# Kernel optimization log

Measured on AMD Instinct MI355X. Metric: run time of the kernel, lower is better.

The kernel has to match this reference:

```python
import jax, jax.numpy as jnp
import numpy as np

SEQ, D, HID, C = 512, 768, 128, 5
NENT, SPAN = 128, 16


def setup_inputs() -> dict:
    key = jax.random.key(0)
    ks = jax.random.split(key, 24)
    s = 0.02

    def rn(k, shape, scale=s):
        return jax.random.normal(k, shape, dtype=jnp.float32) * scale

    inp = {
        "encoder_output": rn(ks[0], (1, SEQ, D), 1.0),
        "holder_idxs": jax.random.randint(ks[1], (NENT, SPAN), 0, SEQ, dtype=jnp.int32),
        "target_idxs": jax.random.randint(ks[2], (NENT, SPAN), 0, SEQ, dtype=jnp.int32),
        "exp_idxs": jax.random.randint(ks[3], (NENT, SPAN), 0, SEQ, dtype=jnp.int32),
    }
    names = ["Wh_f", "bh_f", "Wh_b", "bh_b", "Wt_f", "bt_f", "Wt_b", "bt_b",
             "We_f", "be_f", "We_b", "be_b"]
    for n, k in zip(names, ks[4:16]):
        shape = (4 * HID, D) if n.startswith("W") else (4 * HID,)
        inp[n] = rn(k, shape)
    inp["T_he"] = rn(ks[16], (2 * HID, 2 * HID, 2 * HID))
    inp["T_te"] = rn(ks[17], (2 * HID, 2 * HID, 2 * HID))
    inp["T_cls"] = rn(ks[18], (2 * HID, C, 2 * HID))
    return inp


def _lstm_cell_step(x, W_ih, b):
    # Single LSTM step with h0=c0=0 (the torch module feeds seq_len=1 to nn.LSTM,
    # so W_hh @ h0 vanishes; b = b_ih + b_hh). Gate order: i, f, g, o.
    g = x @ W_ih.T + b                         # [n, L, 4H]
    i, f, gg, o = jnp.split(g, 4, axis=-1)
    c = jax.nn.sigmoid(i) * jnp.tanh(gg)
    return jax.nn.sigmoid(o) * jnp.tanh(c)     # h, [n, L, H]


def _lstm_pool(enc_seq, idxs, Wf, bf, Wb, bb):
    toks = enc_seq[idxs]                       # [n, L, D] gather
    h = jnp.concatenate([_lstm_cell_step(toks, Wf, bf),
                         _lstm_cell_step(toks, Wb, bb)], axis=-1)  # [n, L, 2H]
    return h.max(axis=1)                       # max-pool over span -> [n, 2H]


def reference(encoder_output, holder_idxs, target_idxs, exp_idxs,
              Wh_f, bh_f, Wh_b, bh_b, Wt_f, bt_f, Wt_b, bt_b,
              We_f, be_f, We_b, be_b, T_he, T_te, T_cls):
    enc = encoder_output[0]                    # [SEQ, D]
    He = _lstm_pool(enc, holder_idxs, Wh_f, bh_f, Wh_b, bh_b)   # [nh, 2H]
    Te = _lstm_pool(enc, target_idxs, Wt_f, bt_f, Wt_b, bt_b)   # [nt, 2H]
    Ee = _lstm_pool(enc, exp_idxs, We_f, be_f, We_b, be_b)      # [ne, 2H]

    # hep[i,k] = He[i] @ T_he @ Ee[k];  tep[j,k] = Te[j] @ T_te @ Ee[k]
    hep = jnp.einsum('ia,abc,kc->ikb', He, T_he, Ee)            # [nh, ne, 2H]
    tep = jnp.einsum('ja,abc,kc->jkb', Te, T_te, Ee)            # [nt, ne, 2H]
    # pred[i,j,k,m] = tep[j,k] @ T_cls[:,m,:] @ hep[i,k]
    pred = jnp.einsum('jkb,bmc,ikc->ijkm', tep, T_cls, hep)     # [nh, nt, ne, C]
    return pred
```

## Files before the change

kernel.cpp:

```cpp
#include <hip/hip_runtime.h>
#include <hip/hip_bf16.h>
#include <math.h>

#define DIM   768
#define HID   128
#define H2    256
#define NENT  128
#define SPAN  16
#define NCLS  5

#define POOLB_OFF 0
#define HEPB_OFF  196608
#define TEPB_OFF  (HEPB_OFF + 8388608)
#define TCLSB_OFF (TEPB_OFF + 8388608)
#define WB_OFF    (TCLSB_OFF + 655360)
#define TOKB_OFF  21168128
#define GATES_OFF (TOKB_OFF + 9437184)
#define TMP30_OFF 21168128
#define TMP31_OFF (TMP30_OFF + 16777216)
#define PREDT_OFF 21168128

typedef __attribute__((ext_vector_type(8))) short bf16x8;
typedef __attribute__((ext_vector_type(4))) float f32x4;

__device__ __forceinline__ float sigmoidf_(float x) { return 1.0f / (1.0f + __expf(-x)); }

__device__ __forceinline__ unsigned short f2bf(float x) {
    __hip_bfloat16 h = __float2bfloat16(x);
    return *reinterpret_cast<unsigned short*>(&h);
}

__global__ __launch_bounds__(256)
void prep_kernel(const float* __restrict__ Whf, const float* __restrict__ Whb,
                 const float* __restrict__ Wtf, const float* __restrict__ Wtb,
                 const float* __restrict__ Wef, const float* __restrict__ Web,
                 const float* __restrict__ Tcls, const float* __restrict__ enc,
                 const int* __restrict__ idx_h, const int* __restrict__ idx_t,
                 const int* __restrict__ idx_e,
                 unsigned short* __restrict__ WB, unsigned short* __restrict__ TB,
                 unsigned short* __restrict__ tokB)
{
    const int bb = blockIdx.x;
    const int tid = threadIdx.x;
    if (bb < 1728) {
        int gid = bb * 256 + tid;
        int t2  = gid / 73728;
        int rem = gid % 73728;
        int n   = rem / 192;
        int c4  = rem % 192;
        int gate = n >> 7, j = n & 127;
        int srow = (gate == 0) ? j : (gate == 1) ? 256 + j : 384 + j;
        const float* W = (t2 == 0) ? Whf : (t2 == 1) ? Whb : (t2 == 2) ? Wtf :
                         (t2 == 3) ? Wtb : (t2 == 4) ? Wef : Web;
        float4 v = ((const float4*)(W + srow * DIM))[c4];
        unsigned short* d = WB + ((size_t)(t2 * 384 + n)) * DIM + c4 * 4;
        d[0] = f2bf(v.x); d[1] = f2bf(v.y); d[2] = f2bf(v.z); d[3] = f2bf(v.w);
    } else if (bb < 3008) {
        int idx = (bb - 1728) * 256 + tid;
        int b = idx / (NCLS * H2);
        int r = idx % (NCLS * H2);
        int m = r >> 8, c = r & 255;
        TB[((m << 8) + c) * H2 + b] = f2bf(Tcls[idx]);
    } else {
        int gid = (bb - 3008) * 256 + tid;
        int r  = gid / 192, c4 = gid % 192;
        int type = r >> 11;
        int rem  = r & 2047;
        const int* idx = (type == 0) ? idx_h : (type == 1) ? idx_t : idx_e;
        int row = idx[rem];
        float4 v = ((const float4*)(enc + (size_t)row * DIM))[c4];
        unsigned short h4[4] = { f2bf(v.x), f2bf(v.y), f2bf(v.z), f2bf(v.w) };
        *(uint2*)(tokB + (size_t)r * DIM + c4 * 4) = *(uint2*)h4;
    }
}

__global__ __launch_bounds__(256)
void gates_mfma(const unsigned short* __restrict__ tokB,
                const unsigned short* __restrict__ WB,
                float* __restrict__ gates)
{
    __shared__ unsigned short As[2][128 * 64];
    __shared__ unsigned short Bs[2][128 * 64];
    const int lbid = ((int)blockIdx.x & 7) * 36 + ((int)blockIdx.x >> 3);
    const int type = lbid / 96;
    const int rem  = lbid % 96;
    const int mb0  = (rem / 6) * 128;
    const int nb0  = (rem % 6) * 128;
    const int tid = threadIdx.x;
    const int w = tid >> 6, l = tid & 63;
    const int lr = l & 15, lg = l >> 4;
    const unsigned short* A = tokB + (size_t)type * 2048 * DIM + (size_t)mb0 * DIM;
    const unsigned short* B = WB   + (size_t)type * 768  * DIM + (size_t)nb0 * DIM;

    const int sr0 = tid >> 3;
    const int sc  = tid & 7;

    bf16x8 ra[4], rb[4];
    #define LOADT(kt)                                                        \
        {                                                                    \
            const int koff = (kt) * 64 + sc * 8;                             \
            _Pragma("unroll")                                                \
            for (int p = 0; p < 4; ++p) {                                    \
                int rr = sr0 + p * 32;                                       \
                ra[p] = *(const bf16x8*)(A + (size_t)rr * DIM + koff);       \
                rb[p] = *(const bf16x8*)(B + (size_t)rr * DIM + koff);       \
            }                                                                \
        }
    #define WRITET(buf)                                                      \
        {                                                                    \
            _Pragma("unroll")                                                \
            for (int p = 0; p < 4; ++p) {                                    \
                int rr = sr0 + p * 32;                                       \
                int bo = (rr * 128 + sc * 16) ^ ((rr & 7) << 4);             \
                *(bf16x8*)((char*)As[buf] + bo) = ra[p];                     \
                *(bf16x8*)((char*)Bs[buf] + bo) = rb[p];                     \
            }                                                                \
        }

    f32x4 acc[4][4];
    #pragma unroll
    for (int mt = 0; mt < 4; ++mt)
        #pragma unroll
        for (int nt = 0; nt < 4; ++nt) acc[mt][nt] = (f32x4){0.f, 0.f, 0.f, 0.f};

    const int am0 = (w & 1) * 64;
    const int bn0 = (w >> 1) * 64;

    LOADT(0);
    WRITET(0);
    __syncthreads();

    int cur = 0;
    #pragma unroll 1
    for (int kt = 0; kt < 12; ++kt) {
        if (kt + 1 < 12) LOADT(kt + 1);

        #pragma unroll
        for (int ks = 0; ks < 2; ++ks) {
            bf16x8 af[4], bf[4];
            #pragma unroll
            for (int mt = 0; mt < 4; ++mt) {
                int rr = am0 + mt * 16 + lr;
                int bo = (rr * 128 + ks * 64 + lg * 16) ^ ((rr & 7) << 4);
                af[mt] = *(const bf16x8*)((const char*)As[cur] + bo);
            }
            #pragma unroll
            for (int nt = 0; nt < 4; ++nt) {
                int rr = bn0 + nt * 16 + lr;
                int bo = (rr * 128 + ks * 64 + lg * 16) ^ ((rr & 7) << 4);
                bf[nt] = *(const bf16x8*)((const char*)Bs[cur] + bo);
            }
            #pragma unroll
            for (int mt = 0; mt < 4; ++mt)
                #pragma unroll
                for (int nt = 0; nt < 4; ++nt)
                    acc[mt][nt] = __builtin_amdgcn_mfma_f32_16x16x32_bf16(af[mt], bf[nt], acc[mt][nt], 0, 0, 0);
        }

        if (kt + 1 < 12) {
            WRITET(cur ^ 1);
        }
        __syncthreads();
        cur ^= 1;
    }
    #undef LOADT
    #undef WRITET

    float* C = gates + (size_t)type * 2048 * 768 + (size_t)mb0 * 768 + nb0;
    #pragma unroll
    for (int mt = 0; mt < 4; ++mt)
        #pragma unroll
        for (int nt = 0; nt < 4; ++nt)
            #pragma unroll
            for (int r = 0; r < 4; ++r)
                C[(size_t)(am0 + mt * 16 + lg * 4 + r) * 768 + bn0 + nt * 16 + lr] = acc[mt][nt][r];
}

__global__ __launch_bounds__(256)
void pool_epilogue(const float* __restrict__ gates,
                   const float* __restrict__ bhf, const float* __restrict__ bhb,
                   const float* __restrict__ btf, const float* __restrict__ btb,
                   const float* __restrict__ bef, const float* __restrict__ beb,
                   unsigned short* __restrict__ poolB)
{
    const int type = blockIdx.x >> 7;
    const int ent  = blockIdx.x & 127;
    const int tid  = threadIdx.x;
    const int dir  = tid >> 7;
    const int j    = tid & 127;
    const float* Bv = (type == 0) ? (dir ? bhb : bhf)
                    : (type == 1) ? (dir ? btb : btf)
                                  : (dir ? beb : bef);
    const float bi = Bv[j], bg = Bv[2 * HID + j], bo = Bv[3 * HID + j];
    const float* g0 = gates + ((size_t)type * 2048 + ent * 16) * 768 + dir * 384 + j;
    float hmax = -1e30f;
    #pragma unroll
    for (int l = 0; l < SPAN; ++l) {
        const float* gr = g0 + l * 768;
        float iv = sigmoidf_(gr[0]   + bi);
        float gv = tanhf(   gr[128] + bg);
        float ov = sigmoidf_(gr[256] + bo);
        hmax = fmaxf(hmax, ov * tanhf(iv * gv));
    }
    poolB[(size_t)(type * NENT + ent) * H2 + dir * HID + j] = f2bf(hmax);
}

__global__ __launch_bounds__(1024)
void gemm1_mfma(const unsigned short* __restrict__ EeB,
                const float* __restrict__ T0, const float* __restrict__ T1,
                unsigned short* __restrict__ tmp30, unsigned short* __restrict__ tmp31)
{
    __shared__ __align__(16) char smem[131072];
    const int bid = blockIdx.x;
    const int t = bid >> 8;
    const int a = bid & 255;
    const float* T = t ? T1 : T0;
    unsigned short* outp = t ? tmp31 : tmp30;
    const int tid = threadIdx.x;
    const int w = tid >> 6, l = tid & 63;
    const int lr = l & 15, lg = l >> 4;

    {
        const int r0 = tid >> 5;
        const int ch = tid & 31;
        const float* base = T + (size_t)a * 65536;
        #pragma unroll
        for (int p = 0; p < 8; ++p) {
            int row = p * 32 + r0;
            const float* src = base + row * 256 + ch * 8;
            float4 v0 = ((const float4*)src)[0];
            float4 v1 = ((const float4*)src)[1];
            bf16x8 hv; unsigned short* hp = (unsigned short*)&hv;
            hp[0]=f2bf(v0.x); hp[1]=f2bf(v0.y); hp[2]=f2bf(v0.z); hp[3]=f2bf(v0.w);
            hp[4]=f2bf(v1.x); hp[5]=f2bf(v1.y); hp[6]=f2bf(v1.z); hp[7]=f2bf(v1.w);
            int bo = (row * 512 + ch * 16) ^ ((row & 7) << 4);
            *(bf16x8*)(smem + bo) = hv;
        }
    }
    __syncthreads();

    const int bw = (w & 7) * 32;
    const int kw = (w >> 3) * 64;
    f32x4 acc[2][4];
    #pragma unroll
    for (int mt = 0; mt < 2; ++mt)
        #pragma unroll
        for (int nt = 0; nt < 4; ++nt) acc[mt][nt] = (f32x4){0.f, 0.f, 0.f, 0.f};

    #pragma unroll
    for (int ks = 0; ks < 8; ++ks) {
        bf16x8 af[2], bf[4];
        #pragma unroll
        for (int mt = 0; mt < 2; ++mt) {
            int br = bw + mt * 16 + lr;
            int bo = (br * 512 + (ks * 32 + lg * 8) * 2) ^ ((br & 7) << 4);
            af[mt] = *(const bf16x8*)(smem + bo);
        }
        #pragma unroll
        for (int nt = 0; nt < 4; ++nt)
            bf[nt] = *(const bf16x8*)(EeB + (kw + nt * 16 + lr) * H2 + ks * 32 + lg * 8);
        #pragma unroll
        for (int mt = 0; mt < 2; ++mt)
            #pragma unroll
            for (int nt = 0; nt < 4; ++nt)
                acc[mt][nt] = __builtin_amdgcn_mfma_f32_16x16x32_bf16(af[mt], bf[nt], acc[mt][nt], 0, 0, 0);
    }

    #pragma unroll
    for (int mt = 0; mt < 2; ++mt)
        #pragma unroll
        for (int nt = 0; nt < 4; ++nt)
            #pragma unroll
            for (int r = 0; r < 4; ++r) {
                int b_ = bw + mt * 16 + lg * 4 + r;
                int k_ = kw + nt * 16 + lr;
                outp[((size_t)b_ * 256 + a) * 128 + k_] = f2bf(acc[mt][nt][r]);
            }
}

__global__ __launch_bounds__(512)
void gemm2_mfma(const unsigned short* __restrict__ HeB, const unsigned short* __restrict__ TeB,
                const unsigned short* __restrict__ tmp30, const unsigned short* __restrict__ tmp31,
                unsigned short* __restrict__ hepN, unsigned short* __restrict__ tepN)
{
    __shared__ unsigned short WT[128 * 256];
    const int bid = blockIdx.x;
    const int t = bid >> 8;
    const int b = bid & 255;
    const unsigned short* src = (t ? tmp31 : tmp30) + (size_t)b * 32768;
    const unsigned short* Hx = t ? TeB : HeB;
    unsigned short* outp = (t ? tepN : hepN) + (size_t)b * 16384;
    const int tid = threadIdx.x;
    const int w = tid >> 6, l = tid & 63;
    const int lr = l & 15, lg = l >> 4;

    {
        const int a0 = tid >> 4;
        const int k8 = (tid & 15) * 8;
        #pragma unroll
        for (int it = 0; it < 8; ++it) {
            int aa = it * 32 + a0;
            bf16x8 v = *(const bf16x8*)(src + aa * 128 + k8);
            #pragma unroll
            for (int j = 0; j < 8; ++j) {
                int kk = k8 + j;
                int bo = (kk * 512 + aa * 2) ^ (j << 4);
                *(unsigned short*)((char*)WT + bo) = ((unsigned short*)&v)[j];
            }
        }
    }
    __syncthreads();

    const int kw = (w & 1) * 64;
    const int iw = (w >> 1) * 32;
    f32x4 acc[4][2];
    #pragma unroll
    for (int mt = 0; mt < 4; ++mt)
        #pragma unroll
        for (int nt = 0; nt < 2; ++nt) acc[mt][nt] = (f32x4){0.f, 0.f, 0.f, 0.f};

    #pragma unroll
    for (int ks = 0; ks < 8; ++ks) {
        bf16x8 af[4], bf[2];
        #pragma unroll
        for (int mt = 0; mt < 4; ++mt) {
            int kr = kw + mt * 16 + lr;
            int bo = (kr * 512 + (ks * 32 + lg * 8) * 2) ^ ((kr & 7) << 4);
            af[mt] = *(const bf16x8*)((const char*)WT + bo);
        }
        #pragma unroll
        for (int nt = 0; nt < 2; ++nt)
            bf[nt] = *(const bf16x8*)(Hx + (iw + nt * 16 + lr) * H2 + ks * 32 + lg * 8);
        #pragma unroll
        for (int mt = 0; mt < 4; ++mt)
            #pragma unroll
            for (int nt = 0; nt < 2; ++nt)
                acc[mt][nt] = __builtin_amdgcn_mfma_f32_16x16x32_bf16(af[mt], bf[nt], acc[mt][nt], 0, 0, 0);
    }
    #pragma unroll
    for (int mt = 0; mt < 4; ++mt)
        #pragma unroll
        for (int nt = 0; nt < 2; ++nt)
            #pragma unroll
            for (int r = 0; r < 4; ++r) {
                int k_ = kw + mt * 16 + lg * 4 + r;
                int i_ = iw + nt * 16 + lr;
                outp[k_ * 128 + i_] = f2bf(acc[mt][nt][r]);
            }
}

__global__ __launch_bounds__(512)
void step3_mfma(const unsigned short* __restrict__ hepN,
                const unsigned short* __restrict__ tepN,
                const unsigned short* __restrict__ TclsB,
                float* __restrict__ predT)
{
    __shared__ unsigned short hepS[128 * 256];
    __shared__ unsigned short tepS[64 * 256];
    __shared__ unsigned short WS[64 * 256];
    const int lbid = (blockIdx.x & 7) * 32 + (blockIdx.x >> 3);
    const int k  = lbid >> 1;
    const int jh = lbid & 1;
    const int tid = threadIdx.x;
    const int w  = tid >> 6;
    const int l  = tid & 63;
    const int lr = l & 15;
    const int lg = l >> 4;
    const int swz = (lr & 7) << 4;

    #pragma unroll
    for (int q = 0; q < 4; ++q) {
        int bcol = q * 64 + l;
        bf16x8 v = *(const bf16x8*)(tepN + ((size_t)bcol * 128 + k) * 128 + jh * 64 + w * 8);
        #pragma unroll
        for (int r = 0; r < 8; ++r) {
            int j = w * 8 + r;
            int bo = (j * 512 + bcol * 2) ^ (r << 4);
            *(unsigned short*)((char*)tepS + bo) = ((unsigned short*)&v)[r];
        }
    }
    #pragma unroll
    for (int s = 0; s < 2; ++s)
        #pragma unroll
        for (int q = 0; q < 4; ++q) {
            int bcol = q * 64 + l;
            bf16x8 v = *(const bf16x8*)(hepN + ((size_t)bcol * 128 + k) * 128 + w * 16 + s * 8);
            #pragma unroll
            for (int r = 0; r < 8; ++r) {
                int i = w * 16 + s * 8 + r;
                int bo = (i * 512 + bcol * 2) ^ (r << 4);
                *(unsigned short*)((char*)hepS + bo) = ((unsigned short*)&v)[r];
            }
        }
    __syncthreads();

    bf16x8 ha[8];
    #pragma unroll
    for (int ks = 0; ks < 8; ++ks) {
        int ir = w * 16 + lr;
        int bo = (ir * 512 + (ks * 32 + lg * 8) * 2) ^ ((ir & 7) << 4);
        ha[ks] = *(const bf16x8*)((const char*)hepS + bo);
    }

    #pragma unroll 1
    for (int m = 0; m < NCLS; ++m) {
        {
            const unsigned short* tcm = TclsB + (size_t)m * (H2 * H2);
            f32x4 acc1[4][2];
            #pragma unroll
            for (int jt = 0; jt < 4; ++jt)
                #pragma unroll
                for (int ct = 0; ct < 2; ++ct) acc1[jt][ct] = (f32x4){0.f, 0.f, 0.f, 0.f};

            #pragma unroll
            for (int ks = 0; ks < 8; ++ks) {
                bf16x8 a[4], bb[2];
                #pragma unroll
                for (int jt = 0; jt < 4; ++jt) {
                    int byteoff = ((((jt * 16 + lr) << 8) + ks * 32 + lg * 8) << 1) ^ swz;
                    a[jt] = *(const bf16x8*)((const char*)tepS + byteoff);
                }
                #pragma unroll
                for (int ct = 0; ct < 2; ++ct)
                    bb[ct] = *(const bf16x8*)(tcm + (size_t)(w * 32 + ct * 16 + lr) * H2 + ks * 32 + lg * 8);
                #pragma unroll
                for (int jt = 0; jt < 4; ++jt)
                    #pragma unroll
                    for (int ct = 0; ct < 2; ++ct)
                        acc1[jt][ct] = __builtin_amdgcn_mfma_f32_16x16x32_bf16(a[jt], bb[ct], acc1[jt][ct], 0, 0, 0);
            }
            #pragma unroll
            for (int jt = 0; jt < 4; ++jt)
                #pragma unroll
                for (int ct = 0; ct < 2; ++ct)
                    #pragma unroll
                    for (int r = 0; r < 4; ++r) {
                        int j = jt * 16 + lg * 4 + r;
                        int c = w * 32 + ct * 16 + lr;
                        int byteoff = ((((j << 8) + c)) << 1) ^ ((j & 7) << 4);
                        *(unsigned short*)((char*)WS + byteoff) = f2bf(acc1[jt][ct][r]);
                    }
        }
        __syncthreads();

        {
            f32x4 acc2[4];
            #pragma unroll
            for (int jt = 0; jt < 4; ++jt) acc2[jt] = (f32x4){0.f, 0.f, 0.f, 0.f};

            #pragma unroll
            for (int ks = 0; ks < 8; ++ks) {
                #pragma unroll
                for (int jt = 0; jt < 4; ++jt) {
                    int byteoff = ((((jt * 16 + lr) << 8) + ks * 32 + lg * 8) << 1) ^ swz;
                    bf16x8 wb = *(const bf16x8*)((const char*)WS + byteoff);
                    acc2[jt] = __builtin_amdgcn_mfma_f32_16x16x32_bf16(ha[ks], wb, acc2[jt], 0, 0, 0);
                }
            }
            float* po = predT + (size_t)(k * NCLS + m) * (NENT * NENT);
            #pragma unroll
            for (int jt = 0; jt < 4; ++jt)
                #pragma unroll
                for (int r = 0; r < 4; ++r) {
                    int i = w * 16 + lg * 4 + r;
                    int j = jh * 64 + jt * 16 + lr;
                    po[i * NENT + j] = acc2[jt][r];
                }
        }
        __syncthreads();
    }
}

__global__ __launch_bounds__(256)
void transpose_out(const float* __restrict__ predT, float* __restrict__ out)
{
    __shared__ float Ls[160][33];
    const int bid = blockIdx.x;
    const int ij0 = (bid >> 2) * 32;
    const int km0 = (bid & 3) * 160;
    const int t = threadIdx.x;

    #pragma unroll
    for (int q = 0; q < 20; ++q) {
        int r = (t >> 5) + q * 8;
        int c = t & 31;
        Ls[r][c] = predT[(size_t)(km0 + r) * 16384 + ij0 + c];
    }
    __syncthreads();
    for (int idx = t; idx < 32 * 160; idx += 256) {
        int r = idx / 160, c = idx % 160;
        out[(size_t)(ij0 + r) * 640 + km0 + c] = Ls[c][r];
    }
}

extern "C" void kernel_launch(void* const* d_in, const int* in_sizes, int n_in,
                              void* d_out, int out_size, void* d_ws, size_t ws_size,
                              hipStream_t stream)
{
    (void)in_sizes; (void)n_in; (void)out_size; (void)ws_size;
    const float* enc  = (const float*)d_in[0];
    const int*   hidx = (const int*)d_in[1];
    const int*   tidx = (const int*)d_in[2];
    const int*   eidx = (const int*)d_in[3];
    const float* Whf = (const float*)d_in[4];
    const float* bhf = (const float*)d_in[5];
    const float* Whb = (const float*)d_in[6];
    const float* bhb = (const float*)d_in[7];
    const float* Wtf = (const float*)d_in[8];
    const float* btf = (const float*)d_in[9];
    const float* Wtb = (const float*)d_in[10];
    const float* btb = (const float*)d_in[11];
    const float* Wef = (const float*)d_in[12];
    const float* bef = (const float*)d_in[13];
    const float* Web = (const float*)d_in[14];
    const float* beb = (const float*)d_in[15];
    const float* T_he  = (const float*)d_in[16];
    const float* T_te  = (const float*)d_in[17];
    const float* T_cls = (const float*)d_in[18];

    float* out = (float*)d_out;
    char*  ws  = (char*)d_ws;
    unsigned short* poolB = (unsigned short*)(ws + POOLB_OFF);
    unsigned short* hepN  = (unsigned short*)(ws + HEPB_OFF);
    unsigned short* tepN  = (unsigned short*)(ws + TEPB_OFF);
    unsigned short* TclsB = (unsigned short*)(ws + TCLSB_OFF);
    unsigned short* WB    = (unsigned short*)(ws + WB_OFF);
    unsigned short* tokB  = (unsigned short*)(ws + TOKB_OFF);
    float*          gates = (float*)(ws + GATES_OFF);
    unsigned short* tmp30 = (unsigned short*)(ws + TMP30_OFF);
    unsigned short* tmp31 = (unsigned short*)(ws + TMP31_OFF);
    float*          predT = (float*)(ws + PREDT_OFF);

    unsigned short* HeB = poolB;
    unsigned short* TeB = poolB + 1 * NENT * H2;
    unsigned short* EeB = poolB + 2 * NENT * H2;

    prep_kernel<<<7616, 256, 0, stream>>>(Whf, Whb, Wtf, Wtb, Wef, Web,
                                          T_cls, enc, hidx, tidx, eidx,
                                          WB, TclsB, tokB);

    gates_mfma<<<288, 256, 0, stream>>>(tokB, WB, gates);

    pool_epilogue<<<384, 256, 0, stream>>>(gates, bhf, bhb, btf, btb, bef, beb, poolB);

    gemm1_mfma<<<512, 1024, 0, stream>>>(EeB, T_he, T_te, tmp30, tmp31);

    gemm2_mfma<<<512, 512, 0, stream>>>(HeB, TeB, tmp30, tmp31, hepN, tepN);

    step3_mfma<<<256, 512, 0, stream>>>(hepN, tepN, TclsB, predT);

    transpose_out<<<2048, 256, 0, stream>>>(predT, out);
}
```

Baseline: 168.5 us.

## Store LSTM gates in bf16 and retile first contraction into smaller blocks

```diff
diff --git a/kernel.cpp b/kernel.cpp
--- a/kernel.cpp
+++ b/kernel.cpp
@@ -9,16 +9,16 @@
 #define SPAN  16
 #define NCLS  5
 
-#define POOLB_OFF 0
-#define HEPB_OFF  196608
-#define TEPB_OFF  (HEPB_OFF + 8388608)
-#define TCLSB_OFF (TEPB_OFF + 8388608)
-#define WB_OFF    (TCLSB_OFF + 655360)
-#define TOKB_OFF  21168128
-#define GATES_OFF (TOKB_OFF + 9437184)
-#define TMP30_OFF 21168128
-#define TMP31_OFF (TMP30_OFF + 16777216)
-#define PREDT_OFF 21168128
+#define POOLB_OFF  0
+#define HEPB_OFF   196608
+#define TEPB_OFF   (HEPB_OFF + 8388608)
+#define TCLSB_OFF  (TEPB_OFF + 8388608)
+#define WB_OFF     (TCLSB_OFF + 655360)
+#define TOKB_OFF   21168128
+#define TMP30_OFF  21168128
+#define TMP31_OFF  (TMP30_OFF + 16777216)
+#define GATESB_OFF 58060800
+#define PREDT_OFF  21168128
 
 typedef __attribute__((ext_vector_type(8))) short bf16x8;
 typedef __attribute__((ext_vector_type(4))) float f32x4;
@@ -28,6 +28,10 @@
 __device__ __forceinline__ unsigned short f2bf(float x) {
     __hip_bfloat16 h = __float2bfloat16(x);
     return *reinterpret_cast<unsigned short*>(&h);
+}
+__device__ __forceinline__ float bf2f(unsigned short u) {
+    unsigned int v = ((unsigned int)u) << 16;
+    float f; __builtin_memcpy(&f, &v, 4); return f;
 }
 
 __global__ __launch_bounds__(256)
@@ -77,7 +81,7 @@
 __global__ __launch_bounds__(256)
 void gates_mfma(const unsigned short* __restrict__ tokB,
                 const unsigned short* __restrict__ WB,
-                float* __restrict__ gates)
+                unsigned short* __restrict__ gatesB)
 {
     __shared__ unsigned short As[2][128 * 64];
     __shared__ unsigned short Bs[2][128 * 64];
@@ -166,18 +170,18 @@
     #undef LOADT
     #undef WRITET
 
-    float* C = gates + (size_t)type * 2048 * 768 + (size_t)mb0 * 768 + nb0;
+    unsigned short* C = gatesB + (size_t)type * 2048 * 768 + (size_t)mb0 * 768 + nb0;
     #pragma unroll
     for (int mt = 0; mt < 4; ++mt)
         #pragma unroll
         for (int nt = 0; nt < 4; ++nt)
             #pragma unroll
             for (int r = 0; r < 4; ++r)
-                C[(size_t)(am0 + mt * 16 + lg * 4 + r) * 768 + bn0 + nt * 16 + lr] = acc[mt][nt][r];
+                C[(size_t)(am0 + mt * 16 + lg * 4 + r) * 768 + bn0 + nt * 16 + lr] = f2bf(acc[mt][nt][r]);
 }
 
 __global__ __launch_bounds__(256)
-void pool_epilogue(const float* __restrict__ gates,
+void pool_epilogue(const unsigned short* __restrict__ gatesB,
                    const float* __restrict__ bhf, const float* __restrict__ bhb,
                    const float* __restrict__ btf, const float* __restrict__ btb,
                    const float* __restrict__ bef, const float* __restrict__ beb,
@@ -192,55 +196,53 @@
                     : (type == 1) ? (dir ? btb : btf)
                                   : (dir ? beb : bef);
     const float bi = Bv[j], bg = Bv[2 * HID + j], bo = Bv[3 * HID + j];
-    const float* g0 = gates + ((size_t)type * 2048 + ent * 16) * 768 + dir * 384 + j;
+    const unsigned short* g0 = gatesB + ((size_t)type * 2048 + ent * 16) * 768 + dir * 384 + j;
     float hmax = -1e30f;
     #pragma unroll
-    for (int l = 0; l < SPAN; ++l) {
-        const float* gr = g0 + l * 768;
-        float iv = sigmoidf_(gr[0]   + bi);
-        float gv = tanhf(   gr[128] + bg);
-        float ov = sigmoidf_(gr[256] + bo);
+    for (int ll = 0; ll < SPAN; ++ll) {
+        const unsigned short* gr = g0 + ll * 768;
+        float iv = sigmoidf_(bf2f(gr[0])   + bi);
+        float gv = tanhf(   bf2f(gr[128]) + bg);
+        float ov = sigmoidf_(bf2f(gr[256]) + bo);
         hmax = fmaxf(hmax, ov * tanhf(iv * gv));
     }
     poolB[(size_t)(type * NENT + ent) * H2 + dir * HID + j] = f2bf(hmax);
 }
 
-__global__ __launch_bounds__(1024)
-void gemm1_mfma(const unsigned short* __restrict__ EeB,
-                const float* __restrict__ T0, const float* __restrict__ T1,
-                unsigned short* __restrict__ tmp30, unsigned short* __restrict__ tmp31)
-{
-    __shared__ __align__(16) char smem[131072];
+__global__ __launch_bounds__(256)
+void p1_thin(const unsigned short* __restrict__ EeB,
+             const float* __restrict__ T0, const float* __restrict__ T1,
+             unsigned short* __restrict__ tmp30, unsigned short* __restrict__ tmp31)
+{
+    __shared__ __align__(16) char smem[32768];
     const int bid = blockIdx.x;
-    const int t = bid >> 8;
-    const int a = bid & 255;
+    const int t  = bid >> 10;
+    const int b  = (bid >> 2) & 255;
+    const int aq = bid & 3;
+    const int a0 = aq * 64;
     const float* T = t ? T1 : T0;
     unsigned short* outp = t ? tmp31 : tmp30;
     const int tid = threadIdx.x;
     const int w = tid >> 6, l = tid & 63;
     const int lr = l & 15, lg = l >> 4;
 
-    {
-        const int r0 = tid >> 5;
-        const int ch = tid & 31;
-        const float* base = T + (size_t)a * 65536;
-        #pragma unroll
-        for (int p = 0; p < 8; ++p) {
-            int row = p * 32 + r0;
-            const float* src = base + row * 256 + ch * 8;
-            float4 v0 = ((const float4*)src)[0];
-            float4 v1 = ((const float4*)src)[1];
-            bf16x8 hv; unsigned short* hp = (unsigned short*)&hv;
-            hp[0]=f2bf(v0.x); hp[1]=f2bf(v0.y); hp[2]=f2bf(v0.z); hp[3]=f2bf(v0.w);
-            hp[4]=f2bf(v1.x); hp[5]=f2bf(v1.y); hp[6]=f2bf(v1.z); hp[7]=f2bf(v1.w);
-            int bo = (row * 512 + ch * 16) ^ ((row & 7) << 4);
-            *(bf16x8*)(smem + bo) = hv;
-        }
+    #pragma unroll
+    for (int p = 0; p < 8; ++p) {
+        int L = tid + p * 256;
+        int row = L >> 5, ch = L & 31;
+        const float* src = T + ((size_t)(a0 + row) * 256 + b) * 256 + ch * 8;
+        float4 v0 = ((const float4*)src)[0];
+        float4 v1 = ((const float4*)src)[1];
+        bf16x8 hv; unsigned short* hp = (unsigned short*)&hv;
+        hp[0]=f2bf(v0.x); hp[1]=f2bf(v0.y); hp[2]=f2bf(v0.z); hp[3]=f2bf(v0.w);
+        hp[4]=f2bf(v1.x); hp[5]=f2bf(v1.y); hp[6]=f2bf(v1.z); hp[7]=f2bf(v1.w);
+        int bo = (((ch >> 3) << 13) + row * 128 + ((ch & 7) << 4)) ^ ((row & 7) << 4);
+        *(bf16x8*)(smem + bo) = hv;
     }
     __syncthreads();
 
-    const int bw = (w & 7) * 32;
-    const int kw = (w >> 3) * 64;
+    const int aw = (w & 1) * 32;
+    const int kw = (w >> 1) * 64;
     f32x4 acc[2][4];
     #pragma unroll
     for (int mt = 0; mt < 2; ++mt)
@@ -249,11 +251,12 @@
 
     #pragma unroll
     for (int ks = 0; ks < 8; ++ks) {
+        const int cb = ks * 64 + lg * 16;
         bf16x8 af[2], bf[4];
         #pragma unroll
         for (int mt = 0; mt < 2; ++mt) {
-            int br = bw + mt * 16 + lr;
-            int bo = (br * 512 + (ks * 32 + lg * 8) * 2) ^ ((br & 7) << 4);
+            int row = aw + mt * 16 + lr;
+            int bo = (((cb >> 7) << 13) + row * 128 + (cb & 127)) ^ ((row & 7) << 4);
             af[mt] = *(const bf16x8*)(smem + bo);
         }
         #pragma unroll
@@ -272,9 +275,9 @@
         for (int nt = 0; nt < 4; ++nt)
             #pragma unroll
             for (int r = 0; r < 4; ++r) {
-                int b_ = bw + mt * 16 + lg * 4 + r;
+                int a_ = a0 + aw + mt * 16 + lg * 4 + r;
                 int k_ = kw + nt * 16 + lr;
-                outp[((size_t)b_ * 256 + a) * 128 + k_] = f2bf(acc[mt][nt][r]);
+                outp[((size_t)b * 256 + a_) * 128 + k_] = f2bf(acc[mt][nt][r]);
             }
 }
 
@@ -520,16 +523,16 @@
 
     float* out = (float*)d_out;
     char*  ws  = (char*)d_ws;
-    unsigned short* poolB = (unsigned short*)(ws + POOLB_OFF);
-    unsigned short* hepN  = (unsigned short*)(ws + HEPB_OFF);
-    unsigned short* tepN  = (unsigned short*)(ws + TEPB_OFF);
-    unsigned short* TclsB = (unsigned short*)(ws + TCLSB_OFF);
-    unsigned short* WB    = (unsigned short*)(ws + WB_OFF);
-    unsigned short* tokB  = (unsigned short*)(ws + TOKB_OFF);
-    float*          gates = (float*)(ws + GATES_OFF);
-    unsigned short* tmp30 = (unsigned short*)(ws + TMP30_OFF);
-    unsigned short* tmp31 = (unsigned short*)(ws + TMP31_OFF);
-    float*          predT = (float*)(ws + PREDT_OFF);
+    unsigned short* poolB  = (unsigned short*)(ws + POOLB_OFF);
+    unsigned short* hepN   = (unsigned short*)(ws + HEPB_OFF);
+    unsigned short* tepN   = (unsigned short*)(ws + TEPB_OFF);
+    unsigned short* TclsB  = (unsigned short*)(ws + TCLSB_OFF);
+    unsigned short* WB     = (unsigned short*)(ws + WB_OFF);
+    unsigned short* tokB   = (unsigned short*)(ws + TOKB_OFF);
+    unsigned short* tmp30  = (unsigned short*)(ws + TMP30_OFF);
+    unsigned short* tmp31  = (unsigned short*)(ws + TMP31_OFF);
+    unsigned short* gatesB = (unsigned short*)(ws + GATESB_OFF);
+    float*          predT  = (float*)(ws + PREDT_OFF);
 
     unsigned short* HeB = poolB;
     unsigned short* TeB = poolB + 1 * NENT * H2;
@@ -539,11 +542,11 @@
                                           T_cls, enc, hidx, tidx, eidx,
                                           WB, TclsB, tokB);
 
-    gates_mfma<<<288, 256, 0, stream>>>(tokB, WB, gates);
-
-    pool_epilogue<<<384, 256, 0, stream>>>(gates, bhf, bhb, btf, btb, bef, beb, poolB);
-
-    gemm1_mfma<<<512, 1024, 0, stream>>>(EeB, T_he, T_te, tmp30, tmp31);
+    gates_mfma<<<288, 256, 0, stream>>>(tokB, WB, gatesB);
+
+    pool_epilogue<<<384, 256, 0, stream>>>(gatesB, bhf, bhb, btf, btb, bef, beb, poolB);
+
+    p1_thin<<<2048, 256, 0, stream>>>(EeB, T_he, T_te, tmp30, tmp31);
 
     gemm2_mfma<<<512, 512, 0, stream>>>(HeB, TeB, tmp30, tmp31, hepN, tepN);
 
```

Measured after the change: 160.0 us. -5.0%, faster.
